# Kernel tuning notes

Measured on AMD Instinct MI355X. Metric: run time of the kernel, lower is better.

The kernel has to match this reference:

```python
import jax, jax.numpy as jnp
import numpy as np
from math import gcd

N_SIG = 2097152   # signal length
L_FILT = 129      # FIR taps


def setup_inputs() -> dict:
    key = jax.random.key(0)
    k1, k2 = jax.random.split(key)
    x = jax.random.normal(k1, (N_SIG,), dtype=jnp.float32)
    h = jax.random.normal(k2, (L_FILT,), dtype=jnp.float32)
    return {"x": x, "h": h, "up": 3, "down": 2}


def _get_start_index(length):
    if length <= 2:
        return 0
    return (length - 1) // 2


def reference(x, h, up, down):
    # Reduce rates by gcd, as in the torch module.
    g = gcd(up, down)
    up, down = up // g, down // g
    if up == 1 and down == 1:
        return x
    N = x.shape[0]
    L = h.shape[0]
    # zero-stuff: x_up[::up] = up * x  (gain `up` matches resample_poly)
    x_up = jnp.zeros(up * N, dtype=x.dtype).at[::up].set(up * x)
    # full FIR convolution, then phase-offset strided downsample
    full = jnp.convolve(x_up, h.astype(x.dtype), mode="full")  # [up*N + L - 1]
    start = _get_start_index(L)
    n_out = -(-(N * up) // down)  # ceil(N*up/down)
    return full[start::down][:n_out]
```

## Files before the change

### kernel.cpp

```cpp
#include <hip/hip_runtime.h>


#define N_SIG   2097152
#define L_FILT  129
#define NTAPS   43
#define G       8
#define BLK     256
#define GROUPS_PER_BLK (BLK * G)
#define TILE_Q  4160
#define TILE_P  (TILE_Q + (TILE_Q / 16) * 4)

__global__ __launch_bounds__(BLK) void poly_kernel(
    const float* __restrict__ x, const float* __restrict__ h,
    float* __restrict__ out, int n_out)
{
    __shared__ float xs[TILE_P];
    __shared__ float hs[L_FILT];

    const int tid = threadIdx.x;
    const int b   = blockIdx.x;

    if (tid < L_FILT) hs[tid] = 3.0f * h[tid];

    const int tb = 4096 * b - 24;

    for (int q4 = tid; q4 < TILE_Q / 4; q4 += BLK) {
        const int gx = tb + 4 * q4;
        float4 v;
        if (gx >= 0 && gx + 3 < N_SIG) {
            v = *(const float4*)(x + gx);
        } else {
            v.x = (gx     >= 0 && gx     < N_SIG) ? x[gx]     : 0.0f;
            v.y = (gx + 1 >= 0 && gx + 1 < N_SIG) ? x[gx + 1] : 0.0f;
            v.z = (gx + 2 >= 0 && gx + 2 < N_SIG) ? x[gx + 2] : 0.0f;
            v.w = (gx + 3 >= 0 && gx + 3 < N_SIG) ? x[gx + 3] : 0.0f;
        }
        const int p = 4 * q4 + 4 * (q4 >> 2);
        *(float4*)(xs + p) = v;
    }
    __syncthreads();

    float w[64];
#pragma unroll
    for (int k = 0; k < 16; ++k) {
        const int p = 20 * tid + 4 * k + 4 * (k >> 2);
        const float4 v = *(const float4*)(xs + p);
        w[4 * k + 0] = v.x; w[4 * k + 1] = v.y;
        w[4 * k + 2] = v.z; w[4 * k + 3] = v.w;
    }

    float acc[3 * G];
#pragma unroll
    for (int k = 0; k < 3 * G; ++k) acc[k] = 0.0f;

#pragma unroll
    for (int i = 0; i < NTAPS; ++i) {
        const float h0 = hs[3 * i + 0];
        const float h1 = hs[3 * i + 1];
        const float h2 = hs[3 * i + 2];
#pragma unroll
        for (int g = 0; g < G; ++g) {
            const float xa = w[45 + 2 * g - i];
            const float xb = w[46 + 2 * g - i];
            acc[3 * g + 0] += xa * h1;
            acc[3 * g + 1] += xb * h0;
            acc[3 * g + 2] += xb * h2;
        }
    }

    const long ob = (long)GROUPS_PER_BLK * b * 3 + (long)(3 * G) * tid;
#pragma unroll
    for (int k = 0; k < 6; ++k) {
        if (ob + 4 * k + 3 < (long)n_out) {
            *(float4*)(out + ob + 4 * k) =
                make_float4(acc[4 * k + 0], acc[4 * k + 1],
                            acc[4 * k + 2], acc[4 * k + 3]);
        }
    }
}

extern "C" void kernel_launch(void* const* d_in, const int* in_sizes, int n_in,
                              void* d_out, int out_size, void* d_ws, size_t ws_size,
                              hipStream_t stream) {
    const float* x = (const float*)d_in[0];
    const float* h = (const float*)d_in[1];
    float* out = (float*)d_out;
    const int blocks = (out_size + 3 * GROUPS_PER_BLK - 1) / (3 * GROUPS_PER_BLK);
    poly_kernel<<<blocks, BLK, 0, stream>>>(x, h, out, out_size);
}
```

Baseline: 83.86 us.

## Halve outputs per thread and stream input windows from LDS in tap chunks

Each thread now computes 4 output groups instead of 8, so there are twice as many blocks. Rather than preloading a 64-element register window, the kernel reloads a small window from shared memory for each chunk of 8 taps, using a new padding scheme, and launch bounds ask for 4 blocks per CU. Filter taps are read straight from global memory instead of a scaled shared copy, and the gain of 3 is applied at the store. The aim is lower register pressure and higher occupancy. The cost is more LDS reads per FMA, scalar LDS stores, and scalar global loads of h inside the loop.

```diff
diff --git a/kernel.cpp b/kernel.cpp
--- a/kernel.cpp
+++ b/kernel.cpp
@@ -4,25 +4,48 @@
 #define N_SIG   2097152
 #define L_FILT  129
 #define NTAPS   43
-#define G       8
+#define G       4
 #define BLK     256
 #define GROUPS_PER_BLK (BLK * G)
-#define TILE_Q  4160
-#define TILE_P  (TILE_Q + (TILE_Q / 16) * 4)
+#define TILE_Q  2112
+#define TILE_P  (TILE_Q + TILE_Q / 8)
 
-__global__ __launch_bounds__(BLK) void poly_kernel(
+template <int U, int R>
+__device__ __forceinline__ void do_chunk(const float* __restrict__ xs,
+                                         const float* __restrict__ h,
+                                         int i0, int tid, float (&acc)[3 * G]) {
+    const int D = 45 - (i0 + U - 1);
+    const int pb = 9 * tid + 9 * (D >> 3) + R;
+    float wz[U + 7];
+#pragma unroll
+    for (int k = 0; k < U + 7; ++k)
+        wz[k] = xs[pb + k + ((R + k) >> 3)];
+#pragma unroll
+    for (int u = 0; u < U; ++u) {
+        const float h0 = h[3 * (i0 + u) + 0];
+        const float h1 = h[3 * (i0 + u) + 1];
+        const float h2 = h[3 * (i0 + u) + 2];
+#pragma unroll
+        for (int g = 0; g < G; ++g) {
+            const float xa = wz[(U - 1 - u) + 2 * g];
+            const float xb = wz[(U - 1 - u) + 2 * g + 1];
+            acc[3 * g + 0] += xa * h1;
+            acc[3 * g + 1] += xb * h0;
+            acc[3 * g + 2] += xb * h2;
+        }
+    }
+}
+
+__global__ __launch_bounds__(BLK, 4) void poly_kernel(
     const float* __restrict__ x, const float* __restrict__ h,
     float* __restrict__ out, int n_out)
 {
     __shared__ float xs[TILE_P];
-    __shared__ float hs[L_FILT];
 
     const int tid = threadIdx.x;
     const int b   = blockIdx.x;
 
-    if (tid < L_FILT) hs[tid] = 3.0f * h[tid];
-
-    const int tb = 4096 * b - 24;
+    const int tb = 2 * GROUPS_PER_BLK * b - 24;
 
     for (int q4 = tid; q4 < TILE_Q / 4; q4 += BLK) {
         const int gx = tb + 4 * q4;
@@ -35,46 +58,28 @@
             v.z = (gx + 2 >= 0 && gx + 2 < N_SIG) ? x[gx + 2] : 0.0f;
             v.w = (gx + 3 >= 0 && gx + 3 < N_SIG) ? x[gx + 3] : 0.0f;
         }
-        const int p = 4 * q4 + 4 * (q4 >> 2);
-        *(float4*)(xs + p) = v;
+        const int q = 4 * q4;
+        const int p = q + (q >> 3);
+        xs[p + 0] = v.x; xs[p + 1] = v.y; xs[p + 2] = v.z; xs[p + 3] = v.w;
     }
     __syncthreads();
-
-    float w[64];
-#pragma unroll
-    for (int k = 0; k < 16; ++k) {
-        const int p = 20 * tid + 4 * k + 4 * (k >> 2);
-        const float4 v = *(const float4*)(xs + p);
-        w[4 * k + 0] = v.x; w[4 * k + 1] = v.y;
-        w[4 * k + 2] = v.z; w[4 * k + 3] = v.w;
-    }
 
     float acc[3 * G];
 #pragma unroll
     for (int k = 0; k < 3 * G; ++k) acc[k] = 0.0f;
 
+#pragma unroll 1
+    for (int i0 = 0; i0 < 40; i0 += 8)
+        do_chunk<8, 6>(xs, h, i0, tid, acc);
+    do_chunk<3, 3>(xs, h, 40, tid, acc);
+
+    const int ob = 3 * GROUPS_PER_BLK * b + 3 * G * tid;
 #pragma unroll
-    for (int i = 0; i < NTAPS; ++i) {
-        const float h0 = hs[3 * i + 0];
-        const float h1 = hs[3 * i + 1];
-        const float h2 = hs[3 * i + 2];
-#pragma unroll
-        for (int g = 0; g < G; ++g) {
-            const float xa = w[45 + 2 * g - i];
-            const float xb = w[46 + 2 * g - i];
-            acc[3 * g + 0] += xa * h1;
-            acc[3 * g + 1] += xb * h0;
-            acc[3 * g + 2] += xb * h2;
-        }
-    }
-
-    const long ob = (long)GROUPS_PER_BLK * b * 3 + (long)(3 * G) * tid;
-#pragma unroll
-    for (int k = 0; k < 6; ++k) {
-        if (ob + 4 * k + 3 < (long)n_out) {
+    for (int k = 0; k < 3; ++k) {
+        if (ob + 4 * k + 3 < n_out) {
             *(float4*)(out + ob + 4 * k) =
-                make_float4(acc[4 * k + 0], acc[4 * k + 1],
-                            acc[4 * k + 2], acc[4 * k + 3]);
+                make_float4(3.0f * acc[4 * k + 0], 3.0f * acc[4 * k + 1],
+                            3.0f * acc[4 * k + 2], 3.0f * acc[4 * k + 3]);
         }
     }
 }
```

Result: faster. 70.44 us (-16.0%).
